# Performance work log

Measured on AMD Instinct MI355X. Metric: run time of the kernel, lower is better.

The kernel has to match this reference:

```python
import jax, jax.numpy as jnp
import numpy as np

N_NODES = 100000


def setup_inputs() -> dict:
    key = jax.random.key(0)
    k1, k2, k3, k4, k5 = jax.random.split(key, 5)
    feat = jax.random.normal(k1, (N_NODES, 128), dtype=jnp.float32)
    src = jax.random.randint(k2, (1600000,), 0, N_NODES, dtype=jnp.int32)
    dst = jax.random.randint(k3, (1600000,), 0, N_NODES, dtype=jnp.int32)
    # Xavier-uniform-like weight init
    limit = float(np.sqrt(6.0 / (128 + 128)))
    weight = jax.random.uniform(k4, (128, 128), minval=-limit, maxval=limit, dtype=jnp.float32)
    bias = jax.random.normal(k5, (128,), dtype=jnp.float32) * 0.0  # zeros per reset_parameters
    return {"feat": feat, "src": src, "dst": dst, "weight": weight, "bias": bias}


def reference(feat, src, dst, weight, bias):
    # copy_u/sum: gather source features along edges, scatter-add into destinations
    agg = jax.ops.segment_sum(feat[src], dst, num_segments=N_NODES)  # [N, in_feats]
    rst = agg @ weight  # [N, out_feats]
    # symmetric-ish degree normalization: in_degree^{-0.5}, clamped at 1
    deg = jax.ops.segment_sum(jnp.ones_like(dst, dtype=feat.dtype), dst, num_segments=N_NODES)
    norm = jnp.clip(deg, 1.0, None) ** -0.5  # [N]
    rst = rst * norm[:, None] + bias
    return rst
```

## Files before the change

kernel.cpp:

```cpp
#include <hip/hip_runtime.h>
#include <hip/hip_bf16.h>

#define CHUNK 1024
#define RR 64
#define PDEPTH 96
#define NSUB 16
#define CAPE 2560
#define SUBWMAX 128
typedef unsigned int uint;
typedef unsigned short ushort;

typedef __bf16 bf16x8 __attribute__((ext_vector_type(8)));
typedef float  f32x4  __attribute__((ext_vector_type(4)));

__device__ __forceinline__ ushort f2bf(float f) {
    const uint u = __float_as_uint(f);
    return (ushort)((u + 0x7fffu + ((u >> 16) & 1u)) >> 16);
}

__global__ __launch_bounds__(256) void partition64(const int* __restrict__ src,
                                                   const int* __restrict__ dst,
                                                   int* __restrict__ gcur,
                                                   uint* __restrict__ staging,
                                                   int cap, int nE, int N) {
    __shared__ uint bins[RR][PDEPTH];
    __shared__ int cnt[RR];
    __shared__ int res[RR];
    const int t  = threadIdx.x;
    const int nb = gridDim.x;
    const int rounds = (nE + nb * 1024 - 1) / (nb * 1024);

    for (int rd = 0; rd < rounds; ++rd) {
        if (t < RR) cnt[t] = 0;
        __syncthreads();

        const int e4 = (rd * nb + blockIdx.x) * 1024 + t * 4;
        int s[4], d[4];
        int nv = 0;
        if (e4 + 3 < nE) {
            const int4 s4 = *reinterpret_cast<const int4*>(src + e4);
            const int4 d4 = *reinterpret_cast<const int4*>(dst + e4);
            s[0] = s4.x; s[1] = s4.y; s[2] = s4.z; s[3] = s4.w;
            d[0] = d4.x; d[1] = d4.y; d[2] = d4.z; d[3] = d4.w;
            nv = 4;
        } else {
            for (int e = e4; e < nE; ++e) { s[nv] = src[e]; d[nv] = dst[e]; ++nv; }
        }
#pragma unroll
        for (int i = 0; i < 4; ++i) {
            if (i < nv) {
                const int r  = (int)(((long long)d[i] * RR) / N);
                const int lo = (int)(((long long)r * N + RR - 1) / RR);
                const uint pk = (uint)s[i] | ((uint)(d[i] - lo) << 17);
                const int pos = atomicAdd(&cnt[r], 1);
                if (pos < PDEPTH) {
                    bins[r][pos] = pk;
                } else {
                    const int gp = atomicAdd(&gcur[r], 1);
                    staging[(size_t)r * cap + gp] = pk;
                }
            }
        }
        __syncthreads();
        if (t < RR) {
            int c = cnt[t];
            c = c < PDEPTH ? c : PDEPTH;
            cnt[t] = c;
            res[t] = (c > 0) ? atomicAdd(&gcur[t], c) : 0;
        }
        __syncthreads();
        {
            const int w    = t >> 6;
            const int lane = t & 63;
            for (int rr = w * 16; rr < w * 16 + 16; ++rr) {
                const int c = cnt[rr];
                const int b = res[rr];
                if (lane < c)
                    staging[(size_t)rr * cap + b + lane] = bins[rr][lane];
                if (c > 64 && lane + 64 < c)
                    staging[(size_t)rr * cap + b + 64 + lane] = bins[rr][64 + lane];
            }
        }
        __syncthreads();
    }
}

__global__ __launch_bounds__(256) void prep_w(const float* __restrict__ w,
                                              ushort* __restrict__ wt) {
    const int idx = blockIdx.x * 256 + threadIdx.x;
    const int k = idx >> 7;
    const int n = idx & 127;
    wt[n * 128 + k] = f2bf(w[k * 128 + n]);
}

#define APITCH 136
__global__ __launch_bounds__(256, 2) void gemm_mfma(const float* __restrict__ feat,
                                                    const ushort* __restrict__ wt,
                                                    ushort* __restrict__ h, int M) {
    __shared__ ushort A_lds[64 * APITCH];
    const int t    = threadIdx.x;
    const int wave = t >> 6;
    const int lane = t & 63;
    const int quad = lane >> 4;
    const int nn   = lane & 15;
    const int row0 = blockIdx.x * 64;

    union UB { uint4 u; bf16x8 b; };
    UB bfrag[8][4];
#pragma unroll
    for (int ct = 0; ct < 8; ++ct)
#pragma unroll
        for (int kc = 0; kc < 4; ++kc)
            bfrag[ct][kc].u = *reinterpret_cast<const uint4*>(
                wt + (ct * 16 + nn) * 128 + kc * 32 + quad * 8);

#pragma unroll
    for (int p = 0; p < 8; ++p) {
        const int idx = p * 256 + t;
        const int row = idx >> 5;
        const int c4  = (idx & 31) * 4;
        const int grow = row0 + row;
        float4 v = make_float4(0.f, 0.f, 0.f, 0.f);
        if (grow < M)
            v = *reinterpret_cast<const float4*>(&feat[(size_t)grow * 128 + c4]);
        const uint2 pk = make_uint2((uint)f2bf(v.x) | ((uint)f2bf(v.y) << 16),
                                    (uint)f2bf(v.z) | ((uint)f2bf(v.w) << 16));
        *reinterpret_cast<uint2*>(&A_lds[row * APITCH + c4]) = pk;
    }
    __syncthreads();

    union UA { uint4 u; bf16x8 b; };
    UA afrag[4];
#pragma unroll
    for (int kc = 0; kc < 4; ++kc)
        afrag[kc].u = *reinterpret_cast<const uint4*>(
            &A_lds[(wave * 16 + nn) * APITCH + kc * 32 + quad * 8]);

    f32x4 acc[8];
#pragma unroll
    for (int ct = 0; ct < 8; ++ct) {
        acc[ct] = (f32x4){0.f, 0.f, 0.f, 0.f};
#pragma unroll
        for (int kc = 0; kc < 4; ++kc)
            acc[ct] = __builtin_amdgcn_mfma_f32_16x16x32_bf16(
                afrag[kc].b, bfrag[ct][kc].b, acc[ct], 0, 0, 0);
    }
    __syncthreads();

#pragma unroll
    for (int ct = 0; ct < 8; ++ct) {
#pragma unroll
        for (int reg = 0; reg < 4; ++reg) {
            const int rl = wave * 16 + quad * 4 + reg;
            A_lds[rl * APITCH + ct * 16 + nn] = f2bf(acc[ct][reg]);
        }
    }
    __syncthreads();

#pragma unroll
    for (int p = 0; p < 4; ++p) {
        const int idx = p * 256 + t;
        const int row = idx >> 4;
        const int c16 = idx & 15;
        const int grow = row0 + row;
        if (grow < M) {
            const uint4 v = *reinterpret_cast<const uint4*>(&A_lds[row * APITCH + c16 * 8]);
            *reinterpret_cast<uint4*>(&h[(size_t)grow * 128 + c16 * 8]) = v;
        }
    }
}

__global__ __launch_bounds__(512, 8) void build_agg(const uint* __restrict__ staging,
                                                    const int* __restrict__ gcur,
                                                    const ushort* __restrict__ h,
                                                    const float* __restrict__ bias,
                                                    float* __restrict__ out, int cap, int N) {
    __shared__ uint epack[CAPE];
    __shared__ int  csr_s[CAPE];
    __shared__ int  hist[SUBWMAX];
    __shared__ int  off_s[SUBWMAX];
    __shared__ int  cur_s[SUBWMAX];
    __shared__ int  sbuf[SUBWMAX];
    __shared__ int  scnt;

    const int t    = threadIdx.x;
    const int bid  = blockIdx.x;
    const int xcd  = bid & 7;
    const int i2   = bid >> 3;
    const int r    = xcd * 8 + (i2 >> 4);
    const int sub  = i2 & (NSUB - 1);

    const int lo   = (int)(((long long)r * N + RR - 1) / RR);
    const int hi   = (int)(((long long)(r + 1) * N + RR - 1) / RR);
    const int W    = hi - lo;
    const int SUBW = (W + NSUB - 1) / NSUB;
    const int nlo  = sub * SUBW;
    const int nhi  = min(W, nlo + SUBW);
    const int SW   = nhi - nlo;
    if (SW <= 0) return;

    const int  cnt_r = gcur[r];
    const uint* ep   = staging + (size_t)r * cap;
    const int  lane  = t & 63;

    if (t == 0) scnt = 0;
    if (t < SUBWMAX) hist[t] = 0;
    __syncthreads();

    const int nall = (cnt_r + 511) & ~511;
    for (int i = t; i < nall; i += 512) {
        uint v = 0;
        bool keep = false;
        if (i < cnt_r) {
            v = ep[i];
            const int ld = (int)(v >> 17);
            keep = (ld >= nlo) && (ld < nhi);
        }
        const unsigned long long m = __ballot(keep);
        const int tot = __popcll(m);
        if (tot) {
            int wb = 0;
            if (lane == 0) wb = atomicAdd(&scnt, tot);
            wb = __shfl(wb, 0);
            if (keep) {
                const int p = wb + __popcll(m & ((1ull << lane) - 1ull));
                if (p < CAPE) epack[p] = v;
            }
        }
    }
    __syncthreads();
    const int ne = min(scnt, CAPE);

    for (int i = t; i < ne; i += 512)
        atomicAdd(&hist[(int)(epack[i] >> 17) - nlo], 1);
    __syncthreads();

    int v0 = 0;
    if (t < SUBWMAX) { v0 = hist[t]; sbuf[t] = v0; }
    __syncthreads();
    for (int d = 1; d < SUBWMAX; d <<= 1) {
        int x = 0;
        if (t < SUBWMAX && t >= d) x = sbuf[t - d];
        __syncthreads();
        if (t < SUBWMAX) sbuf[t] += x;
        __syncthreads();
    }
    if (t < SUBWMAX) { const int e = sbuf[t] - v0; off_s[t] = e; cur_s[t] = e; }
    __syncthreads();

    for (int i = t; i < ne; i += 512) {
        const uint v  = epack[i];
        const int ld  = (int)(v >> 17) - nlo;
        const int pos = atomicAdd(&cur_s[ld], 1);
        csr_s[pos] = (int)(v & 0x1FFFFu);
    }
    __syncthreads();

    const int wv  = t >> 6;
    const int q   = lane >> 4;
    const int sbl = lane & 15;

#define UNPACK_ADD(rr)                                             \
    do {                                                           \
        acc[0] += __uint_as_float(((rr).x & 0xffffu) << 16);       \
        acc[1] += __uint_as_float((rr).x & 0xffff0000u);           \
        acc[2] += __uint_as_float(((rr).y & 0xffffu) << 16);       \
        acc[3] += __uint_as_float((rr).y & 0xffff0000u);           \
        acc[4] += __uint_as_float(((rr).z & 0xffffu) << 16);       \
        acc[5] += __uint_as_float((rr).z & 0xffff0000u);           \
        acc[6] += __uint_as_float(((rr).w & 0xffffu) << 16);       \
        acc[7] += __uint_as_float((rr).w & 0xffff0000u);           \
    } while (0)

    for (int n = wv; n < SW; n += 8) {
        const int start = off_s[n];
        const int dg    = hist[n];
        const int end   = start + dg;

        float acc[8];
#pragma unroll
        for (int k = 0; k < 8; ++k) acc[k] = 0.0f;

        int j = start;
        for (; j + 15 < end; j += 16) {
            int s[4];
#pragma unroll
            for (int k = 0; k < 4; ++k) s[k] = csr_s[j + q + 4 * k];
            uint4 rg[4];
#pragma unroll
            for (int k = 0; k < 4; ++k)
                rg[k] = *reinterpret_cast<const uint4*>(h + (size_t)s[k] * 128 + sbl * 8);
#pragma unroll
            for (int k = 0; k < 4; ++k) UNPACK_ADD(rg[k]);
        }
        for (; j + 3 < end; j += 4) {
            const int s = csr_s[j + q];
            const uint4 rr = *reinterpret_cast<const uint4*>(h + (size_t)s * 128 + sbl * 8);
            UNPACK_ADD(rr);
        }
        const int rem = end - j;
        if (q < rem) {
            const int s = csr_s[j + q];
            const uint4 rr = *reinterpret_cast<const uint4*>(h + (size_t)s * 128 + sbl * 8);
            UNPACK_ADD(rr);
        }

#pragma unroll
        for (int k = 0; k < 8; ++k) {
            acc[k] += __shfl_xor(acc[k], 16, 64);
            acc[k] += __shfl_xor(acc[k], 32, 64);
        }

        if (lane < 16) {
            const float nm = rsqrtf(fmaxf((float)dg, 1.0f));
            const float4 b0 = *reinterpret_cast<const float4*>(bias + sbl * 8 + 0);
            const float4 b1 = *reinterpret_cast<const float4*>(bias + sbl * 8 + 4);
            float4 o0, o1;
            o0.x = fmaf(acc[0], nm, b0.x);
            o0.y = fmaf(acc[1], nm, b0.y);
            o0.z = fmaf(acc[2], nm, b0.z);
            o0.w = fmaf(acc[3], nm, b0.w);
            o1.x = fmaf(acc[4], nm, b1.x);
            o1.y = fmaf(acc[5], nm, b1.y);
            o1.z = fmaf(acc[6], nm, b1.z);
            o1.w = fmaf(acc[7], nm, b1.w);
            const size_t gnode = (size_t)(lo + nlo + n);
            *reinterpret_cast<float4*>(out + gnode * 128 + sbl * 8 + 0) = o0;
            *reinterpret_cast<float4*>(out + gnode * 128 + sbl * 8 + 4) = o1;
        }
    }
#undef UNPACK_ADD
}

__global__ void hist_simple(const int* __restrict__ dst, int* __restrict__ deg, int nE) {
    int e = blockIdx.x * blockDim.x + threadIdx.x;
    if (e < nE) atomicAdd(&deg[dst[e]], 1);
}
__global__ void bucket_simple(const int* __restrict__ src, const int* __restrict__ dst,
                              int* __restrict__ cur, int* __restrict__ csr, int nE) {
    int e = blockIdx.x * blockDim.x + threadIdx.x;
    if (e < nE) {
        int pos = atomicAdd(&cur[dst[e]], 1);
        csr[pos] = src[e];
    }
}
__global__ __launch_bounds__(256) void scan_chunks(const int* __restrict__ deg,
                                                   int* __restrict__ off,
                                                   int* __restrict__ partials, int N) {
    __shared__ int sums[256];
    const int b = blockIdx.x, t = threadIdx.x;
    const int base = b * CHUNK + t * 4;
    int v[4];
#pragma unroll
    for (int i = 0; i < 4; ++i) v[i] = (base + i < N) ? deg[base + i] : 0;
    const int s = v[0] + v[1] + v[2] + v[3];
    sums[t] = s;
    __syncthreads();
    for (int d = 1; d < 256; d <<= 1) {
        int x = (t >= d) ? sums[t - d] : 0;
        __syncthreads();
        sums[t] += x;
        __syncthreads();
    }
    const int excl = sums[t] - s;
    if (t == 255) partials[b] = sums[255];
    int run = excl;
#pragma unroll
    for (int i = 0; i < 4; ++i) {
        if (base + i < N) off[base + i] = run;
        run += v[i];
    }
}
__global__ __launch_bounds__(256) void scan_partials(int* partials, int P) {
    __shared__ int buf[256];
    const int t = threadIdx.x;
    if (P <= 256) {
        const int v = (t < P) ? partials[t] : 0;
        buf[t] = v;
        __syncthreads();
        for (int d = 1; d < 256; d <<= 1) {
            int x = (t >= d) ? buf[t - d] : 0;
            __syncthreads();
            buf[t] += x;
            __syncthreads();
        }
        if (t < P) partials[t] = buf[t] - v;
    } else if (t == 0) {
        int acc = 0;
        for (int i = 0; i < P; ++i) { int v = partials[i]; partials[i] = acc; acc += v; }
    }
}
__global__ void add_base(int* __restrict__ off, int* __restrict__ cur,
                         const int* __restrict__ partials, int N) {
    int i = blockIdx.x * blockDim.x + threadIdx.x;
    if (i < N) {
        int o = off[i] + partials[i >> 10];
        off[i] = o;
        cur[i] = o;
    }
}
__global__ __launch_bounds__(256) void aggregate_f32(const float* __restrict__ feat,
                                                     const int* __restrict__ csr,
                                                     const int* __restrict__ off,
                                                     const int* __restrict__ deg,
                                                     float* __restrict__ out, int N) {
    const int node = (blockIdx.x * blockDim.x + threadIdx.x) >> 6;
    if (node >= N) return;
    const int lane = threadIdx.x & 63;
    const int start = off[node];
    const int end   = start + deg[node];
    const float2* feat2 = reinterpret_cast<const float2*>(feat);
    float ax = 0.0f, ay = 0.0f;
    for (int j = start; j < end; ++j) {
        const float2 v = feat2[(size_t)csr[j] * 64 + lane];
        ax += v.x;
        ay += v.y;
    }
    reinterpret_cast<float2*>(out)[(size_t)node * 64 + lane] = make_float2(ax, ay);
}
__global__ __launch_bounds__(256) void gemm_norm(const float* agg,
                                                 const float* __restrict__ weight,
                                                 const float* __restrict__ bias,
                                                 const int* __restrict__ deg,
                                                 float* out, int M) {
    __shared__ float As[64][68];
    __shared__ float Wc[64][128];
    const int t  = threadIdx.x;
    const int tx = t & 15;
    const int ty = t >> 4;
    const int row0 = blockIdx.x * 64;
    float acc[4][8];
#pragma unroll
    for (int i = 0; i < 4; ++i)
#pragma unroll
        for (int j = 0; j < 8; ++j) acc[i][j] = 0.0f;
    for (int c = 0; c < 2; ++c) {
        if (c) __syncthreads();
        {
            const int k4 = (t & 15) * 4;
            const int rbase = t >> 4;
#pragma unroll
            for (int p = 0; p < 4; ++p) {
                const int rr = rbase + p * 16;
                const int grow = row0 + rr;
                float4 v = make_float4(0.f, 0.f, 0.f, 0.f);
                if (grow < M)
                    v = *reinterpret_cast<const float4*>(&agg[(size_t)grow * 128 + c * 64 + k4]);
                *reinterpret_cast<float4*>(&As[rr][k4]) = v;
            }
        }
        {
#pragma unroll
            for (int p = 0; p < 8; ++p) {
                const int idx = (p * 256 + t) * 4;
                const int kk = idx >> 7;
                const int j = idx & 127;
                *reinterpret_cast<float4*>(&Wc[kk][j]) =
                    *reinterpret_cast<const float4*>(&weight[(c * 64 + kk) * 128 + j]);
            }
        }
        __syncthreads();
#pragma unroll 8
        for (int k = 0; k < 64; ++k) {
            float a[4];
#pragma unroll
            for (int i = 0; i < 4; ++i) a[i] = As[ty * 4 + i][k];
            const float4 b0 = *reinterpret_cast<const float4*>(&Wc[k][tx * 8 + 0]);
            const float4 b1 = *reinterpret_cast<const float4*>(&Wc[k][tx * 8 + 4]);
            const float b[8] = {b0.x, b0.y, b0.z, b0.w, b1.x, b1.y, b1.z, b1.w};
#pragma unroll
            for (int i = 0; i < 4; ++i)
#pragma unroll
                for (int j = 0; j < 8; ++j)
                    acc[i][j] = fmaf(a[i], b[j], acc[i][j]);
        }
    }
    float bcol[8];
#pragma unroll
    for (int j = 0; j < 8; ++j) bcol[j] = bias[tx * 8 + j];
#pragma unroll
    for (int i = 0; i < 4; ++i) {
        const int grow = row0 + ty * 4 + i;
        if (grow < M) {
            const float nm = rsqrtf(fmaxf((float)deg[grow], 1.0f));
            float4 o0, o1;
            o0.x = fmaf(acc[i][0], nm, bcol[0]);
            o0.y = fmaf(acc[i][1], nm, bcol[1]);
            o0.z = fmaf(acc[i][2], nm, bcol[2]);
            o0.w = fmaf(acc[i][3], nm, bcol[3]);
            o1.x = fmaf(acc[i][4], nm, bcol[4]);
            o1.y = fmaf(acc[i][5], nm, bcol[5]);
            o1.z = fmaf(acc[i][6], nm, bcol[6]);
            o1.w = fmaf(acc[i][7], nm, bcol[7]);
            *reinterpret_cast<float4*>(&out[(size_t)grow * 128 + tx * 8 + 0]) = o0;
            *reinterpret_cast<float4*>(&out[(size_t)grow * 128 + tx * 8 + 4]) = o1;
        }
    }
}

extern "C" void kernel_launch(void* const* d_in, const int* in_sizes, int n_in,
                              void* d_out, int out_size, void* d_ws, size_t ws_size,
                              hipStream_t stream) {
    const float* feat   = (const float*)d_in[0];
    const int*   src    = (const int*)d_in[1];
    const int*   dst    = (const int*)d_in[2];
    const float* weight = (const float*)d_in[3];
    const float* bias   = (const float*)d_in[4];
    float* out = (float*)d_out;

    const int nE = in_sizes[1];
    const int M  = in_sizes[0] / 128;
    const int P  = (M + CHUNK - 1) / CHUNK;

    int*    gcur    = (int*)d_ws;
    ushort* wt      = (ushort*)(gcur + RR);
    uint*   staging = (uint*)(wt + 16384);
    const int cap = (((nE + RR - 1) / RR + 8192) + 3) & ~3;
    ushort* h = (ushort*)(staging + (size_t)RR * cap);
    const size_t need = (size_t)RR * 4 + 32768 + (size_t)RR * cap * 4 + (size_t)M * 128 * 2;

    if (ws_size >= need && M <= 131072) {
        hipMemsetAsync(gcur, 0, RR * sizeof(int), stream);
        prep_w<<<64, 256, 0, stream>>>(weight, wt);
        gemm_mfma<<<(M + 63) / 64, 256, 0, stream>>>(feat, wt, h, M);
        partition64<<<1024, 256, 0, stream>>>(src, dst, gcur, staging, cap, nE, M);
        build_agg<<<RR * NSUB, 512, 0, stream>>>(staging, gcur, h, bias, out, cap, M);
    } else {
        int* degi     = (int*)d_ws;
        int* off      = degi + M;
        int* cur      = off + M;
        int* partials = cur + M;
        int* csr      = partials + 256;
        hipMemsetAsync(degi, 0, (size_t)M * sizeof(int), stream);
        hist_simple<<<(nE + 255) / 256, 256, 0, stream>>>(dst, degi, nE);
        scan_chunks<<<P, 256, 0, stream>>>(degi, off, partials, M);
        scan_partials<<<1, 256, 0, stream>>>(partials, P);
        add_base<<<(M + 255) / 256, 256, 0, stream>>>(off, cur, partials, M);
        bucket_simple<<<(nE + 255) / 256, 256, 0, stream>>>(src, dst, cur, csr, nE);
        aggregate_f32<<<(M + 3) / 4, 256, 0, stream>>>(feat, csr, off, degi, out, M);
        gemm_norm<<<(M + 63) / 64, 256, 0, stream>>>(out, weight, bias, degi, out, M);
    }
}
```

Before: 249.3 us.

## Split partition staging into per-segment slices and interleave two nodes per wave

The partition kernel now spreads each range's global atomic counter and staging buffer across 8 segments chosen by block index, so blocks contend on separate counters. The aggregation kernel reads all 8 segment slices per range. Each wave in the gather loop now works on two destination nodes at once, giving more independent loads in flight. Bias loads are hoisted out of the node loop. The cost is extra segment loops, a smaller per-segment capacity with a possible overflow risk under skewed inputs, and higher register pressure.

```diff
diff --git a/kernel.cpp b/kernel.cpp
--- a/kernel.cpp
+++ b/kernel.cpp
@@ -3,6 +3,7 @@
 
 #define CHUNK 1024
 #define RR 64
+#define NSEG 8
 #define PDEPTH 96
 #define NSUB 16
 #define CAPE 2560
@@ -22,12 +23,13 @@
                                                    const int* __restrict__ dst,
                                                    int* __restrict__ gcur,
                                                    uint* __restrict__ staging,
-                                                   int cap, int nE, int N) {
+                                                   int capseg, int nE, int N) {
     __shared__ uint bins[RR][PDEPTH];
     __shared__ int cnt[RR];
     __shared__ int res[RR];
-    const int t  = threadIdx.x;
-    const int nb = gridDim.x;
+    const int t   = threadIdx.x;
+    const int nb  = gridDim.x;
+    const int seg = blockIdx.x & (NSEG - 1);
     const int rounds = (nE + nb * 1024 - 1) / (nb * 1024);
 
     for (int rd = 0; rd < rounds; ++rd) {
@@ -56,8 +58,8 @@
                 if (pos < PDEPTH) {
                     bins[r][pos] = pk;
                 } else {
-                    const int gp = atomicAdd(&gcur[r], 1);
-                    staging[(size_t)r * cap + gp] = pk;
+                    const int gp = atomicAdd(&gcur[r * NSEG + seg], 1);
+                    staging[(size_t)(r * NSEG + seg) * capseg + gp] = pk;
                 }
             }
         }
@@ -66,7 +68,7 @@
             int c = cnt[t];
             c = c < PDEPTH ? c : PDEPTH;
             cnt[t] = c;
-            res[t] = (c > 0) ? atomicAdd(&gcur[t], c) : 0;
+            res[t] = (c > 0) ? atomicAdd(&gcur[t * NSEG + seg], c) : 0;
         }
         __syncthreads();
         {
@@ -75,10 +77,9 @@
             for (int rr = w * 16; rr < w * 16 + 16; ++rr) {
                 const int c = cnt[rr];
                 const int b = res[rr];
-                if (lane < c)
-                    staging[(size_t)rr * cap + b + lane] = bins[rr][lane];
-                if (c > 64 && lane + 64 < c)
-                    staging[(size_t)rr * cap + b + 64 + lane] = bins[rr][64 + lane];
+                uint* sp = staging + (size_t)(rr * NSEG + seg) * capseg + b;
+                if (lane < c) sp[lane] = bins[rr][lane];
+                if (c > 64 && lane + 64 < c) sp[64 + lane] = bins[rr][64 + lane];
             }
         }
         __syncthreads();
@@ -174,7 +175,8 @@
                                                     const int* __restrict__ gcur,
                                                     const ushort* __restrict__ h,
                                                     const float* __restrict__ bias,
-                                                    float* __restrict__ out, int cap, int N) {
+                                                    float* __restrict__ out,
+                                                    int capseg, int N) {
     __shared__ uint epack[CAPE];
     __shared__ int  csr_s[CAPE];
     __shared__ int  hist[SUBWMAX];
@@ -199,32 +201,34 @@
     const int SW   = nhi - nlo;
     if (SW <= 0) return;
 
-    const int  cnt_r = gcur[r];
-    const uint* ep   = staging + (size_t)r * cap;
-    const int  lane  = t & 63;
+    const int lane = t & 63;
 
     if (t == 0) scnt = 0;
     if (t < SUBWMAX) hist[t] = 0;
     __syncthreads();
 
-    const int nall = (cnt_r + 511) & ~511;
-    for (int i = t; i < nall; i += 512) {
-        uint v = 0;
-        bool keep = false;
-        if (i < cnt_r) {
-            v = ep[i];
-            const int ld = (int)(v >> 17);
-            keep = (ld >= nlo) && (ld < nhi);
-        }
-        const unsigned long long m = __ballot(keep);
-        const int tot = __popcll(m);
-        if (tot) {
-            int wb = 0;
-            if (lane == 0) wb = atomicAdd(&scnt, tot);
-            wb = __shfl(wb, 0);
-            if (keep) {
-                const int p = wb + __popcll(m & ((1ull << lane) - 1ull));
-                if (p < CAPE) epack[p] = v;
+    for (int s8 = 0; s8 < NSEG; ++s8) {
+        const int  cseg = gcur[r * NSEG + s8];
+        const uint* ep  = staging + (size_t)(r * NSEG + s8) * capseg;
+        const int  nall = (cseg + 511) & ~511;
+        for (int i = t; i < nall; i += 512) {
+            uint v = 0;
+            bool keep = false;
+            if (i < cseg) {
+                v = ep[i];
+                const int ld = (int)(v >> 17);
+                keep = (ld >= nlo) && (ld < nhi);
+            }
+            const unsigned long long m = __ballot(keep);
+            const int tot = __popcll(m);
+            if (tot) {
+                int wb = 0;
+                if (lane == 0) wb = atomicAdd(&scnt, tot);
+                wb = __shfl(wb, 0);
+                if (keep) {
+                    const int p = wb + __popcll(m & ((1ull << lane) - 1ull));
+                    if (p < CAPE) epack[p] = v;
+                }
             }
         }
     }
@@ -259,8 +263,10 @@
     const int wv  = t >> 6;
     const int q   = lane >> 4;
     const int sbl = lane & 15;
-
-#define UNPACK_ADD(rr)                                             \
+    const float4 bias0 = *reinterpret_cast<const float4*>(bias + sbl * 8 + 0);
+    const float4 bias1 = *reinterpret_cast<const float4*>(bias + sbl * 8 + 4);
+
+#define UNPACK_ADD(acc, rr)                                        \
     do {                                                           \
         acc[0] += __uint_as_float(((rr).x & 0xffffu) << 16);       \
         acc[1] += __uint_as_float((rr).x & 0xffff0000u);           \
@@ -272,63 +278,99 @@
         acc[7] += __uint_as_float((rr).w & 0xffff0000u);           \
     } while (0)
 
-    for (int n = wv; n < SW; n += 8) {
-        const int start = off_s[n];
-        const int dg    = hist[n];
-        const int end   = start + dg;
-
-        float acc[8];
-#pragma unroll
-        for (int k = 0; k < 8; ++k) acc[k] = 0.0f;
-
-        int j = start;
-        for (; j + 15 < end; j += 16) {
-            int s[4];
-#pragma unroll
-            for (int k = 0; k < 4; ++k) s[k] = csr_s[j + q + 4 * k];
-            uint4 rg[4];
-#pragma unroll
-            for (int k = 0; k < 4; ++k)
-                rg[k] = *reinterpret_cast<const uint4*>(h + (size_t)s[k] * 128 + sbl * 8);
-#pragma unroll
-            for (int k = 0; k < 4; ++k) UNPACK_ADD(rg[k]);
-        }
-        for (; j + 3 < end; j += 4) {
-            const int s = csr_s[j + q];
-            const uint4 rr = *reinterpret_cast<const uint4*>(h + (size_t)s * 128 + sbl * 8);
-            UNPACK_ADD(rr);
-        }
-        const int rem = end - j;
-        if (q < rem) {
-            const int s = csr_s[j + q];
-            const uint4 rr = *reinterpret_cast<const uint4*>(h + (size_t)s * 128 + sbl * 8);
-            UNPACK_ADD(rr);
-        }
-
-#pragma unroll
-        for (int k = 0; k < 8; ++k) {
-            acc[k] += __shfl_xor(acc[k], 16, 64);
-            acc[k] += __shfl_xor(acc[k], 32, 64);
-        }
-
-        if (lane < 16) {
-            const float nm = rsqrtf(fmaxf((float)dg, 1.0f));
-            const float4 b0 = *reinterpret_cast<const float4*>(bias + sbl * 8 + 0);
-            const float4 b1 = *reinterpret_cast<const float4*>(bias + sbl * 8 + 4);
-            float4 o0, o1;
-            o0.x = fmaf(acc[0], nm, b0.x);
-            o0.y = fmaf(acc[1], nm, b0.y);
-            o0.z = fmaf(acc[2], nm, b0.z);
-            o0.w = fmaf(acc[3], nm, b0.w);
-            o1.x = fmaf(acc[4], nm, b1.x);
-            o1.y = fmaf(acc[5], nm, b1.y);
-            o1.z = fmaf(acc[6], nm, b1.z);
-            o1.w = fmaf(acc[7], nm, b1.w);
-            const size_t gnode = (size_t)(lo + nlo + n);
-            *reinterpret_cast<float4*>(out + gnode * 128 + sbl * 8 + 0) = o0;
-            *reinterpret_cast<float4*>(out + gnode * 128 + sbl * 8 + 4) = o1;
-        }
-    }
+#define LOAD16(rg, jj)                                                           \
+    do {                                                                         \
+        const int s0_ = csr_s[(jj) + q];                                         \
+        const int s1_ = csr_s[(jj) + q + 4];                                     \
+        const int s2_ = csr_s[(jj) + q + 8];                                     \
+        const int s3_ = csr_s[(jj) + q + 12];                                    \
+        rg[0] = *reinterpret_cast<const uint4*>(h + (size_t)s0_ * 128 + sbl * 8);\
+        rg[1] = *reinterpret_cast<const uint4*>(h + (size_t)s1_ * 128 + sbl * 8);\
+        rg[2] = *reinterpret_cast<const uint4*>(h + (size_t)s2_ * 128 + sbl * 8);\
+        rg[3] = *reinterpret_cast<const uint4*>(h + (size_t)s3_ * 128 + sbl * 8);\
+    } while (0)
+
+#define ADD16(acc, rg)                                             \
+    do {                                                           \
+        UNPACK_ADD(acc, rg[0]);                                    \
+        UNPACK_ADD(acc, rg[1]);                                    \
+        UNPACK_ADD(acc, rg[2]);                                    \
+        UNPACK_ADD(acc, rg[3]);                                    \
+    } while (0)
+
+#define TAIL4(acc, jj, ee)                                                           \
+    do {                                                                             \
+        for (; (jj) + 3 < (ee); (jj) += 4) {                                         \
+            const int s_ = csr_s[(jj) + q];                                          \
+            const uint4 rr_ = *reinterpret_cast<const uint4*>(                       \
+                h + (size_t)s_ * 128 + sbl * 8);                                     \
+            UNPACK_ADD(acc, rr_);                                                    \
+        }                                                                            \
+        if (q < (ee) - (jj)) {                                                       \
+            const int s_ = csr_s[(jj) + q];                                          \
+            const uint4 rr_ = *reinterpret_cast<const uint4*>(                       \
+                h + (size_t)s_ * 128 + sbl * 8);                                     \
+            UNPACK_ADD(acc, rr_);                                                    \
+        }                                                                            \
+    } while (0)
+
+#define REDUCE_STORE(acc, nn, dgv)                                                   \
+    do {                                                                             \
+        _Pragma("unroll")                                                            \
+        for (int k = 0; k < 8; ++k) {                                                \
+            acc[k] += __shfl_xor(acc[k], 16, 64);                                    \
+            acc[k] += __shfl_xor(acc[k], 32, 64);                                    \
+        }                                                                            \
+        if (lane < 16) {                                                             \
+            const float nm = rsqrtf(fmaxf((float)(dgv), 1.0f));                      \
+            float4 o0, o1;                                                           \
+            o0.x = fmaf(acc[0], nm, bias0.x);                                        \
+            o0.y = fmaf(acc[1], nm, bias0.y);                                        \
+            o0.z = fmaf(acc[2], nm, bias0.z);                                        \
+            o0.w = fmaf(acc[3], nm, bias0.w);                                        \
+            o1.x = fmaf(acc[4], nm, bias1.x);                                        \
+            o1.y = fmaf(acc[5], nm, bias1.y);                                        \
+            o1.z = fmaf(acc[6], nm, bias1.z);                                        \
+            o1.w = fmaf(acc[7], nm, bias1.w);                                        \
+            const size_t gnode = (size_t)(lo + nlo + (nn));                          \
+            *reinterpret_cast<float4*>(out + gnode * 128 + sbl * 8 + 0) = o0;        \
+            *reinterpret_cast<float4*>(out + gnode * 128 + sbl * 8 + 4) = o1;        \
+        }                                                                            \
+    } while (0)
+
+    for (int n0 = wv; n0 < SW; n0 += 16) {
+        const int n1   = n0 + 8;
+        const bool hasB = (n1 < SW);
+        int jA = off_s[n0];
+        const int dgA = hist[n0];
+        const int endA = jA + dgA;
+        int jB = 0, endB = 0, dgB = 0;
+        if (hasB) { jB = off_s[n1]; dgB = hist[n1]; endB = jB + dgB; }
+
+        float accA[8], accB[8];
+#pragma unroll
+        for (int k = 0; k < 8; ++k) { accA[k] = 0.0f; accB[k] = 0.0f; }
+
+        while ((jA + 15 < endA) && (jB + 15 < endB)) {
+            uint4 ra[4], rb[4];
+            LOAD16(ra, jA);
+            LOAD16(rb, jB);
+            ADD16(accA, ra);
+            ADD16(accB, rb);
+            jA += 16; jB += 16;
+        }
+        for (; jA + 15 < endA; jA += 16) { uint4 ra[4]; LOAD16(ra, jA); ADD16(accA, ra); }
+        for (; jB + 15 < endB; jB += 16) { uint4 rb[4]; LOAD16(rb, jB); ADD16(accB, rb); }
+        TAIL4(accA, jA, endA);
+        if (hasB) TAIL4(accB, jB, endB);
+
+        REDUCE_STORE(accA, n0, dgA);
+        if (hasB) REDUCE_STORE(accB, n1, dgB);
+    }
+#undef REDUCE_STORE
+#undef TAIL4
+#undef ADD16
+#undef LOAD16
 #undef UNPACK_ADD
 }
 
@@ -513,18 +555,19 @@
     const int P  = (M + CHUNK - 1) / CHUNK;
 
     int*    gcur    = (int*)d_ws;
-    ushort* wt      = (ushort*)(gcur + RR);
+    ushort* wt      = (ushort*)(gcur + RR * NSEG);
     uint*   staging = (uint*)(wt + 16384);
-    const int cap = (((nE + RR - 1) / RR + 8192) + 3) & ~3;
-    ushort* h = (ushort*)(staging + (size_t)RR * cap);
-    const size_t need = (size_t)RR * 4 + 32768 + (size_t)RR * cap * 4 + (size_t)M * 128 * 2;
+    const int capseg = ((nE / (RR * NSEG)) + 1024 + 3) & ~3;
+    ushort* h = (ushort*)(staging + (size_t)RR * NSEG * capseg);
+    const size_t need = (size_t)RR * NSEG * 4 + 32768 +
+                        (size_t)RR * NSEG * capseg * 4 + (size_t)M * 128 * 2;
 
     if (ws_size >= need && M <= 131072) {
-        hipMemsetAsync(gcur, 0, RR * sizeof(int), stream);
+        hipMemsetAsync(gcur, 0, RR * NSEG * sizeof(int), stream);
         prep_w<<<64, 256, 0, stream>>>(weight, wt);
         gemm_mfma<<<(M + 63) / 64, 256, 0, stream>>>(feat, wt, h, M);
-        partition64<<<1024, 256, 0, stream>>>(src, dst, gcur, staging, cap, nE, M);
-        build_agg<<<RR * NSUB, 512, 0, stream>>>(staging, gcur, h, bias, out, cap, M);
+        partition64<<<1024, 256, 0, stream>>>(src, dst, gcur, staging, capseg, nE, M);
+        build_agg<<<RR * NSUB, 512, 0, stream>>>(staging, gcur, h, bias, out, capseg, M);
     } else {
         int* degi     = (int*)d_ws;
         int* off      = degi + M;
```

New measurement: 317.9 us. +27.5%, slower.
